# Performance work log

Hardware: AMD Instinct MI355X
Metric: run time of the kernel (lower is better)

Reference implementation:

```python
import jax, jax.numpy as jnp
import numpy as np

B = 2048   # batch
D = 1280   # backbone feature dim (hardcoded in module)
E = 8      # num_classes == number of expert heads
ALPHA = 0.1
EPS = 1e-5


def _bn(x, g, b, m, v):
    # BatchNorm1d in eval mode: running stats
    return (x - m) * jax.lax.rsqrt(v + EPS) * g + b


def _ln(x, g, b):
    mu = jnp.mean(x, axis=-1, keepdims=True)
    var = jnp.mean((x - mu) ** 2, axis=-1, keepdims=True)
    return (x - mu) * jax.lax.rsqrt(var + EPS) * g + b


@jax.custom_vjp
def _grad_reverse(x):
    return x

def _gr_fwd(x):
    return x, None

def _gr_bwd(_, g):
    return (-ALPHA * g,)

_grad_reverse.defvjp(_gr_fwd, _gr_bwd)


def setup_inputs() -> dict:
    key = jax.random.key(0)
    ks = iter(jax.random.split(key, 80))
    def w(*s):
        return jax.random.normal(next(ks), s, dtype=jnp.float32) * 0.02
    def u(*s):
        return jax.random.uniform(next(ks), s, dtype=jnp.float32) + 0.5
    inp = {"source": jax.random.normal(next(ks), (B, D), dtype=jnp.float32)}
    # bottleneck: Linear(1280,512)+BN+ReLU, Linear(512,256)+BN+ReLU
    inp.update(bw1=w(D, 512), bb1=jnp.zeros(512), bg1=jnp.ones(512), bbe1=jnp.zeros(512), bm1=w(512), bv1=u(512))
    inp.update(bw2=w(512, 256), bb2=jnp.zeros(256), bg2=jnp.ones(256), bbe2=jnp.zeros(256), bm2=w(256), bv2=u(256))
    # source_fc: Linear(256, E) + LogSoftmax
    inp.update(cw=w(256, E), cb=jnp.zeros(E))
    # domain classifier: 1280->1024->1024->512->2 with BN
    inp.update(dw1=w(D, 1024), db1=jnp.zeros(1024), dg1=jnp.ones(1024), dbe1=jnp.zeros(1024), dm1=w(1024), dv1=u(1024))
    inp.update(dw2=w(1024, 1024), db2=jnp.zeros(1024), dg2=jnp.ones(1024), dbe2=jnp.zeros(1024), dm2=w(1024), dv2=u(1024))
    inp.update(dw3=w(1024, 512), db3=jnp.zeros(512), dg3=jnp.ones(512), dbe3=jnp.zeros(512), dm3=w(512), dv3=u(512))
    inp.update(dw4=w(512, 2), db4=jnp.zeros(2))
    # E stacked expert MLPs: 1280->1024->1024->512->2 with LayerNorm
    inp.update(ew1=w(E, D, 1024), eb1=jnp.zeros((E, 1024)), eg1=jnp.ones((E, 1024)), ebe1=jnp.zeros((E, 1024)))
    inp.update(ew2=w(E, 1024, 1024), eb2=jnp.zeros((E, 1024)), eg2=jnp.ones((E, 1024)), ebe2=jnp.zeros((E, 1024)))
    inp.update(ew3=w(E, 1024, 512), eb3=jnp.zeros((E, 512)), eg3=jnp.ones((E, 512)), ebe3=jnp.zeros((E, 512)))
    inp.update(ew4=w(E, 512, 2), eb4=jnp.zeros((E, 2)))
    return inp


def reference(source, bw1, bb1, bg1, bbe1, bm1, bv1, bw2, bb2, bg2, bbe2, bm2, bv2, cw, cb,
              dw1, db1, dg1, dbe1, dm1, dv1, dw2, db2, dg2, dbe2, dm2, dv2,
              dw3, db3, dg3, dbe3, dm3, dv3, dw4, db4,
              ew1, eb1, eg1, ebe1, ew2, eb2, eg2, ebe2, ew3, eb3, eg3, ebe3, ew4, eb4):
    share = source  # sharedNet modeled as identity on extracted features
    # bottleneck + classifier head
    h = jax.nn.relu(_bn(share @ bw1 + bb1, bg1, bbe1, bm1, bv1))
    h = jax.nn.relu(_bn(h @ bw2 + bb2, bg2, bbe2, bm2, bv2))
    src = jax.nn.log_softmax(h @ cw + cb, axis=-1)            # [B, E]
    label = jnp.argmax(src, axis=-1)                          # routing labels (detached by argmax)
    # gradient-reversed features
    rev = _grad_reverse(share)
    # global domain classifier (dropout = identity in eval)
    d = jax.nn.relu(_bn(rev @ dw1 + db1, dg1, dbe1, dm1, dv1))
    d = jax.nn.relu(_bn(d @ dw2 + db2, dg2, dbe2, dm2, dv2))
    d = jax.nn.relu(_bn(d @ dw3 + db3, dg3, dbe3, dm3, dv3))
    dclf = jax.nn.log_softmax(d @ dw4 + db4, axis=-1)         # [B, 2]
    # per-class domain experts: dense all-expert compute + per-sample gather
    x = jax.nn.relu(_ln(jnp.einsum('bd,edh->beh', rev, ew1) + eb1[None], eg1[None], ebe1[None]))
    x = jax.nn.relu(_ln(jnp.einsum('beh,ehk->bek', x, ew2) + eb2[None], eg2[None], ebe2[None]))
    x = jax.nn.relu(_ln(jnp.einsum('beh,ehk->bek', x, ew3) + eb3[None], eg3[None], ebe3[None]))
    eo = jax.nn.log_softmax(jnp.einsum('beh,ehk->bek', x, ew4) + eb4[None], axis=-1)  # [B, E, 2]
    sout = jnp.take_along_axis(eo, label[:, None, None], axis=1)[:, 0, :]             # [B, 2]
    return (src, dclf, sout, share)
```

## Files before the change

### kernel.cpp

```cpp
#include <hip/hip_runtime.h>

typedef unsigned short u16;
typedef short s8v __attribute__((ext_vector_type(8)));
typedef float f4v __attribute__((ext_vector_type(4)));

#define AS1 __attribute__((address_space(1)))
#define AS3 __attribute__((address_space(3)))

__device__ __forceinline__ float bf2f(u16 u) {
    union { unsigned int i; float f; } x; x.i = ((unsigned int)u) << 16; return x.f;
}
__device__ __forceinline__ u16 f2bf(float f) {
    union { float f; unsigned int i; } x; x.f = f;
    unsigned int r = x.i + 0x7fffu + ((x.i >> 16) & 1u);
    return (u16)(r >> 16);
}

__device__ __forceinline__ void glds16(const u16* g, u16* l) {
    __builtin_amdgcn_global_load_lds((AS1 void*)(g), (AS3 void*)(l), 16, 0, 0);
}

__global__ __launch_bounds__(256) void convT_k(const float* __restrict__ W,
        u16* __restrict__ WT, int N, int K)
{
    const size_t mat = (size_t)blockIdx.z * K * N;
    const int n0 = blockIdx.x * 64, k0 = blockIdx.y * 64;
    __shared__ float t[64][65];
    const int r = threadIdx.x >> 2;
    const int c = (threadIdx.x & 3) << 4;
    const float* wp = W + mat + (size_t)(k0 + r) * N + n0 + c;
    #pragma unroll
    for (int q = 0; q < 16; q += 4) {
        float4 f = *(const float4*)(wp + q);
        t[c + q + 0][r] = f.x; t[c + q + 1][r] = f.y;
        t[c + q + 2][r] = f.z; t[c + q + 3][r] = f.w;
    }
    __syncthreads();
    u16* op = WT + mat + (size_t)(n0 + r) * K + k0 + c;
    #pragma unroll
    for (int q = 0; q < 16; q += 8) {
        s8v v;
        #pragma unroll
        for (int j = 0; j < 8; ++j) v[j] = (short)f2bf(t[r][c + q + j]);
        *(s8v*)(op + q) = v;
    }
}

__global__ __launch_bounds__(256) void conv_k(const float* __restrict__ in,
        u16* __restrict__ out, int n8)
{
    const int i = blockIdx.x * 256 + threadIdx.x;
    if (i >= n8) return;
    const float4 f0 = ((const float4*)in)[i * 2];
    const float4 f1 = ((const float4*)in)[i * 2 + 1];
    s8v v;
    v[0]=(short)f2bf(f0.x); v[1]=(short)f2bf(f0.y);
    v[2]=(short)f2bf(f0.z); v[3]=(short)f2bf(f0.w);
    v[4]=(short)f2bf(f1.x); v[5]=(short)f2bf(f1.y);
    v[6]=(short)f2bf(f1.z); v[7]=(short)f2bf(f1.w);
    ((s8v*)out)[i] = v;
}

template<int HASDOM>
__global__ __launch_bounds__(256) void gemm_bt128_k(
    const u16* __restrict__ A0, size_t aStrideZ,
    const u16* __restrict__ WT0,
    const float* __restrict__ ebias,
    const float* __restrict__ dbias, const float* __restrict__ dgam,
    const float* __restrict__ dbet,  const float* __restrict__ dmean,
    const float* __restrict__ dvar,  int zdom,
    u16* __restrict__ out0, int M, int N, int K)
{
    const int z = blockIdx.z;
    const u16* A  = A0  + (size_t)z * aStrideZ;
    const u16* WT = WT0 + (size_t)z * N * K;
    u16* out = out0 + (size_t)z * M * N;

    const int n0 = blockIdx.x * 128, m0 = blockIdx.y * 128;
    const int t = threadIdx.x;
    const int w = t >> 6, lane = t & 63;
    const int lq = lane >> 4, lr = lane & 15;
    const int wm = (w >> 1) * 64, wn = (w & 1) * 64;

    __shared__ __align__(16) u16 As[128 * 64];
    __shared__ __align__(16) u16 Bs[128 * 64];

    f4v acc[4][4] = {};

    const u16* ga = A  + (size_t)(m0 + (t >> 3)) * K + ((t & 7) << 3);
    const u16* gb = WT + (size_t)(n0 + (t >> 3)) * K + ((t & 7) << 3);
    const int ldsb = w * 512;

    for (int kk = 0; kk < K; kk += 64) {
        #pragma unroll
        for (int q = 0; q < 4; ++q) {
            glds16(ga + kk + (size_t)q * 32 * K, &As[q * 2048 + ldsb]);
            glds16(gb + kk + (size_t)q * 32 * K, &Bs[q * 2048 + ldsb]);
        }
        __syncthreads();
        #pragma unroll
        for (int ks = 0; ks < 64; ks += 32) {
            const int kq = ks + (lq << 3);
            s8v a[4], b[4];
            #pragma unroll
            for (int i = 0; i < 4; ++i) a[i] = *(const s8v*)&As[(wm + i*16 + lr) * 64 + kq];
            #pragma unroll
            for (int j = 0; j < 4; ++j) b[j] = *(const s8v*)&Bs[(wn + j*16 + lr) * 64 + kq];
            #pragma unroll
            for (int i = 0; i < 4; ++i)
                #pragma unroll
                for (int j = 0; j < 4; ++j)
                    acc[i][j] = __builtin_amdgcn_mfma_f32_16x16x32_bf16(a[i], b[j], acc[i][j], 0, 0, 0);
        }
        __syncthreads();
    }

    float scale[4], shift[4];
    const bool dom = HASDOM && (z == zdom);
    #pragma unroll
    for (int j = 0; j < 4; ++j) {
        const int c = n0 + wn + j * 16 + lr;
        if (dom) {
            const float s = dgam[c] / sqrtf(dvar[c] + 1e-5f);
            scale[j] = s;
            shift[j] = (dbias[c] - dmean[c]) * s + dbet[c];
        } else {
            scale[j] = 1.f;
            shift[j] = ebias[(size_t)z * N + c];
        }
    }
    const int r0 = lq << 2;
    #pragma unroll
    for (int i = 0; i < 4; ++i) {
        #pragma unroll
        for (int r = 0; r < 4; ++r) {
            const int grow = m0 + wm + i * 16 + r0 + r;
            u16* orow = out + (size_t)grow * N + n0 + wn + lr;
            #pragma unroll
            for (int j = 0; j < 4; ++j) {
                float y = fmaf(acc[i][j][r], scale[j], shift[j]);
                if (dom) y = fmaxf(y, 0.f);
                orow[j * 16] = f2bf(y);
            }
        }
    }
}

__global__ __launch_bounds__(256) void gemm_f32sk_k(
    const float* __restrict__ A, const float* __restrict__ W,
    float* __restrict__ out, int M, int N, int K, int Ks)
{
    const int n0 = blockIdx.x * 64, m0 = blockIdx.y * 64;
    const int kb = blockIdx.z * Ks;
    out += (size_t)blockIdx.z * M * N;
    const int tid = threadIdx.x;
    const int tx = tid & 15, ty = tid >> 4;
    __shared__ float As[64][65];
    __shared__ float Bs[64][64];
    float acc[4][4] = {};
    const int sr = tid >> 2;
    const int sc = (tid & 3) << 4;
    for (int kk = kb; kk < kb + Ks; kk += 64) {
        const float* ap = A + (size_t)(m0 + sr) * K + kk + sc;
        #pragma unroll
        for (int q = 0; q < 4; ++q) {
            float4 f = *(const float4*)(ap + q * 4);
            As[sr][sc + q*4 + 0] = f.x; As[sr][sc + q*4 + 1] = f.y;
            As[sr][sc + q*4 + 2] = f.z; As[sr][sc + q*4 + 3] = f.w;
        }
        const float* wp = W + (size_t)(kk + sr) * N + n0 + sc;
        #pragma unroll
        for (int q = 0; q < 4; ++q)
            *(float4*)&Bs[sr][sc + q*4] = *(const float4*)(wp + q * 4);
        __syncthreads();
        #pragma unroll 4
        for (int kq = 0; kq < 64; ++kq) {
            float a[4], bv[4];
            #pragma unroll
            for (int i = 0; i < 4; ++i) a[i] = As[ty*4 + i][kq];
            #pragma unroll
            for (int j = 0; j < 4; ++j) bv[j] = Bs[kq][tx*4 + j];
            #pragma unroll
            for (int i = 0; i < 4; ++i)
                #pragma unroll
                for (int j = 0; j < 4; ++j)
                    acc[i][j] = fmaf(a[i], bv[j], acc[i][j]);
        }
        __syncthreads();
    }
    #pragma unroll
    for (int j = 0; j < 4; ++j) {
        const int c = n0 + tx*4 + j;
        #pragma unroll
        for (int i = 0; i < 4; ++i)
            out[(size_t)(m0 + ty*4 + i) * N + c] = acc[i][j];
    }
}

__global__ __launch_bounds__(256) void h2cls_k(
    const float* __restrict__ hp,
    const float* __restrict__ bb1, const float* __restrict__ bg1,
    const float* __restrict__ bbe1, const float* __restrict__ bm1,
    const float* __restrict__ bv1,
    const float* __restrict__ bw2, const float* __restrict__ bb2,
    const float* __restrict__ bg2, const float* __restrict__ bbe2,
    const float* __restrict__ bm2, const float* __restrict__ bv2,
    const float* __restrict__ cw,  const float* __restrict__ cb,
    float* __restrict__ out_src, int* __restrict__ label, int B)
{
    const int b0 = blockIdx.x * 4;
    const int t = threadIdx.x;
    const size_t sl = (size_t)B * 512;
    __shared__ float h1s[4][512];
    __shared__ float h2s[4][256];

    #pragma unroll
    for (int cc = 0; cc < 2; ++cc) {
        const int c = t + cc * 256;
        const float sc = bg1[c] / sqrtf(bv1[c] + 1e-5f);
        const float sh = (bb1[c] - bm1[c]) * sc + bbe1[c];
        #pragma unroll
        for (int s = 0; s < 4; ++s) {
            const size_t ix = (size_t)(b0 + s) * 512 + c;
            const float v = hp[ix] + hp[ix + sl] + hp[ix + 2*sl] + hp[ix + 3*sl];
            h1s[s][c] = fmaxf(fmaf(v, sc, sh), 0.f);
        }
    }
    __syncthreads();

    float acc[4] = {};
    #pragma unroll 4
    for (int k = 0; k < 512; ++k) {
        const float wv = bw2[(size_t)k * 256 + t];
        #pragma unroll
        for (int s = 0; s < 4; ++s) acc[s] = fmaf(h1s[s][k], wv, acc[s]);
    }
    const float sc2 = bg2[t] / sqrtf(bv2[t] + 1e-5f);
    const float sh2 = (bb2[t] - bm2[t]) * sc2 + bbe2[t];
    #pragma unroll
    for (int s = 0; s < 4; ++s) h2s[s][t] = fmaxf(fmaf(acc[s], sc2, sh2), 0.f);
    __syncthreads();

    const int s = t >> 6, lane = t & 63;
    float p[8] = {};
    for (int k = lane; k < 256; k += 64) {
        const float x = h2s[s][k];
        #pragma unroll
        for (int c = 0; c < 8; ++c) p[c] = fmaf(x, cw[k * 8 + c], p[c]);
    }
    #pragma unroll
    for (int off = 32; off; off >>= 1)
        #pragma unroll
        for (int c = 0; c < 8; ++c) p[c] += __shfl_xor(p[c], off, 64);
    if (lane == 0) {
        const int b = b0 + s;
        float lg[8];
        #pragma unroll
        for (int c = 0; c < 8; ++c) lg[c] = p[c] + cb[c];
        float mx = lg[0]; int am = 0;
        #pragma unroll
        for (int c = 1; c < 8; ++c) if (lg[c] > mx) { mx = lg[c]; am = c; }
        float ssum = 0.f;
        #pragma unroll
        for (int c = 0; c < 8; ++c) ssum += expf(lg[c] - mx);
        const float lse = mx + logf(ssum);
        #pragma unroll
        for (int c = 0; c < 8; ++c) out_src[b * 8 + c] = lg[c] - lse;
        label[b] = am;
    }
}

template<int N>
__global__ __launch_bounds__(256) void ln_relu_k(u16* __restrict__ Y,
        const float* __restrict__ g, const float* __restrict__ bb)
{
    const int z = blockIdx.y;
    u16* y = Y + ((size_t)z * gridDim.x + blockIdx.x) * N;
    const float* gz = g  + (size_t)z * N;
    const float* bz = bb + (size_t)z * N;
    const int t = threadIdx.x;
    constexpr int C = N >> 8;
    float vals[C];
    if (C == 4) {
        ushort4 u = ((const ushort4*)y)[t];
        vals[0] = bf2f(u.x); vals[1] = bf2f(u.y);
        vals[2] = bf2f(u.z); vals[3] = bf2f(u.w);
    } else {
        ushort2 u = ((const ushort2*)y)[t];
        vals[0] = bf2f(u.x); vals[1] = bf2f(u.y);
    }
    float s = 0.f, sq = 0.f;
    #pragma unroll
    for (int i = 0; i < C; ++i) { s += vals[i]; sq += vals[i] * vals[i]; }
    #pragma unroll
    for (int off = 32; off; off >>= 1) {
        s  += __shfl_xor(s,  off, 64);
        sq += __shfl_xor(sq, off, 64);
    }
    __shared__ float rs[4], rq[4];
    if ((t & 63) == 0) { rs[t >> 6] = s; rq[t >> 6] = sq; }
    __syncthreads();
    s  = rs[0] + rs[1] + rs[2] + rs[3];
    sq = rq[0] + rq[1] + rq[2] + rq[3];
    const float inv = 1.f / (float)N;
    const float mu  = s * inv;
    const float var = sq * inv - mu * mu;
    const float rstd = rsqrtf(var + 1e-5f);
    if (C == 4) {
        float4 gv = ((const float4*)gz)[t];
        float4 bv = ((const float4*)bz)[t];
        ushort4 o;
        o.x = f2bf(fmaxf((vals[0] - mu) * rstd * gv.x + bv.x, 0.f));
        o.y = f2bf(fmaxf((vals[1] - mu) * rstd * gv.y + bv.y, 0.f));
        o.z = f2bf(fmaxf((vals[2] - mu) * rstd * gv.z + bv.z, 0.f));
        o.w = f2bf(fmaxf((vals[3] - mu) * rstd * gv.w + bv.w, 0.f));
        ((ushort4*)y)[t] = o;
    } else {
        float2 gv = ((const float2*)gz)[t];
        float2 bv = ((const float2*)bz)[t];
        ushort2 o;
        o.x = f2bf(fmaxf((vals[0] - mu) * rstd * gv.x + bv.x, 0.f));
        o.y = f2bf(fmaxf((vals[1] - mu) * rstd * gv.y + bv.y, 0.f));
        ((ushort2*)y)[t] = o;
    }
}

__global__ __launch_bounds__(64) void head2_k(const u16* __restrict__ X, size_t xsz,
        const float* __restrict__ W, size_t wsz,
        const float* __restrict__ bias, size_t bsz,
        int K, float* __restrict__ out, size_t osz)
{
    const int b = blockIdx.x, z = blockIdx.y;
    const int lane = threadIdx.x;
    const u16* x = X + z * xsz + (size_t)b * K;
    const float* Wz = W + z * wsz;
    const float* bz = bias + z * bsz;
    float* o = out + z * osz + (size_t)b * 2;
    float p0 = 0.f, p1 = 0.f;
    for (int k = lane; k < K; k += 64) {
        const float xv = bf2f(x[k]);
        p0 = fmaf(xv, Wz[k * 2],     p0);
        p1 = fmaf(xv, Wz[k * 2 + 1], p1);
    }
    #pragma unroll
    for (int off = 32; off; off >>= 1) {
        p0 += __shfl_xor(p0, off, 64);
        p1 += __shfl_xor(p1, off, 64);
    }
    if (lane == 0) {
        const float l0 = p0 + bz[0];
        const float l1 = p1 + bz[1];
        const float mx = fmaxf(l0, l1);
        const float lse = mx + logf(expf(l0 - mx) + expf(l1 - mx));
        o[0] = l0 - lse;
        o[1] = l1 - lse;
    }
}

__global__ __launch_bounds__(256) void gather_k(const float* __restrict__ eo,
        const int* __restrict__ label, float* __restrict__ out, int B)
{
    const int b = blockIdx.x * 256 + threadIdx.x;
    if (b >= B) return;
    const int e = label[b];
    out[b * 2]     = eo[((size_t)e * B + b) * 2];
    out[b * 2 + 1] = eo[((size_t)e * B + b) * 2 + 1];
}

__global__ __launch_bounds__(256) void copy16_k(const uint4* __restrict__ in,
                                                uint4* __restrict__ out, int n16)
{
    const int i = blockIdx.x * blockDim.x + threadIdx.x;
    if (i < n16) out[i] = in[i];
}


extern "C" void kernel_launch(void* const* d_in, const int* in_sizes, int n_in,
                              void* d_out, int out_size, void* d_ws, size_t ws_size,
                              hipStream_t stream)
{
    const int B = 2048, D = 1280, E = 8;

    const float* src = (const float*)d_in[0];
    const float *bw1 = (const float*)d_in[1],  *bb1 = (const float*)d_in[2],
                *bg1 = (const float*)d_in[3],  *bbe1 = (const float*)d_in[4],
                *bm1 = (const float*)d_in[5],  *bv1 = (const float*)d_in[6];
    const float *bw2 = (const float*)d_in[7],  *bb2 = (const float*)d_in[8],
                *bg2 = (const float*)d_in[9],  *bbe2 = (const float*)d_in[10],
                *bm2 = (const float*)d_in[11], *bv2 = (const float*)d_in[12];
    const float *cw  = (const float*)d_in[13], *cb  = (const float*)d_in[14];
    const float *dw1 = (const float*)d_in[15], *db1 = (const float*)d_in[16],
                *dg1 = (const float*)d_in[17], *dbe1 = (const float*)d_in[18],
                *dm1 = (const float*)d_in[19], *dv1 = (const float*)d_in[20];
    const float *dw2 = (const float*)d_in[21], *db2 = (const float*)d_in[22],
                *dg2 = (const float*)d_in[23], *dbe2 = (const float*)d_in[24],
                *dm2 = (const float*)d_in[25], *dv2 = (const float*)d_in[26];
    const float *dw3 = (const float*)d_in[27], *db3 = (const float*)d_in[28],
                *dg3 = (const float*)d_in[29], *dbe3 = (const float*)d_in[30],
                *dm3 = (const float*)d_in[31], *dv3 = (const float*)d_in[32];
    const float *dw4 = (const float*)d_in[33], *db4 = (const float*)d_in[34];
    const float *ew1 = (const float*)d_in[35], *eb1 = (const float*)d_in[36],
                *eg1 = (const float*)d_in[37], *ebe1 = (const float*)d_in[38];
    const float *ew2 = (const float*)d_in[39], *eb2 = (const float*)d_in[40],
                *eg2 = (const float*)d_in[41], *ebe2 = (const float*)d_in[42];
    const float *ew3 = (const float*)d_in[43], *eb3 = (const float*)d_in[44],
                *eg3 = (const float*)d_in[45], *ebe3 = (const float*)d_in[46];
    const float *ew4 = (const float*)d_in[47], *eb4 = (const float*)d_in[48];

    float* out_src   = (float*)d_out;
    float* out_dclf  = out_src + B * E;
    float* out_sout  = out_dclf + B * 2;
    float* out_share = out_sout + B * 2;

    char* ws = (char*)d_ws;
    u16*   wslot = (u16*)ws;
    u16*   srcb  = (u16*)(ws + 13107200);
    u16*   acta  = (u16*)(ws + 18350080);
    u16*   actb  = (u16*)(ws + 39321600);
    float* eo    = (float*)(ws + 60293120);
    int*   label = (int*)(ws + 60424192);
    float* hp    = (float*)(ws + 18350080);

    const size_t s1024 = (size_t)B * 1024, s512 = (size_t)B * 512;

    conv_k<<<dim3(B * D / 8 / 256), 256, 0, stream>>>(src, srcb, B * D / 8);
    copy16_k<<<dim3(B * D * 4 / 16 / 256), 256, 0, stream>>>(
        (const uint4*)src, (uint4*)out_share, B * D * 4 / 16);

    gemm_f32sk_k<<<dim3(512 / 64, B / 64, 4), 256, 0, stream>>>(
        src, bw1, hp, B, 512, D, 320);
    h2cls_k<<<dim3(B / 4), 256, 0, stream>>>(
        hp, bb1, bg1, bbe1, bm1, bv1, bw2, bb2, bg2, bbe2, bm2, bv2,
        cw, cb, out_src, label, B);

    convT_k<<<dim3(16, 20, 4), 256, 0, stream>>>(ew1, wslot, 1024, 1280);
    convT_k<<<dim3(16, 20, 1), 256, 0, stream>>>(dw1, wslot + (size_t)4*1024*1280, 1024, 1280);
    gemm_bt128_k<1><<<dim3(8, 16, 5), 256, 0, stream>>>(
        srcb, 0, wslot, eb1, db1, dg1, dbe1, dm1, dv1, 4, acta, B, 1024, 1280);
    ln_relu_k<1024><<<dim3(B, 4), 256, 0, stream>>>(acta, eg1, ebe1);

    convT_k<<<dim3(16, 16, 4), 256, 0, stream>>>(ew2, wslot, 1024, 1024);
    convT_k<<<dim3(16, 16, 1), 256, 0, stream>>>(dw2, wslot + (size_t)4*1024*1024, 1024, 1024);
    gemm_bt128_k<1><<<dim3(8, 16, 5), 256, 0, stream>>>(
        acta, s1024, wslot, eb2, db2, dg2, dbe2, dm2, dv2, 4, actb, B, 1024, 1024);
    ln_relu_k<1024><<<dim3(B, 4), 256, 0, stream>>>(actb, eg2, ebe2);

    convT_k<<<dim3(8, 16, 4), 256, 0, stream>>>(ew3, wslot, 512, 1024);
    convT_k<<<dim3(8, 16, 1), 256, 0, stream>>>(dw3, wslot + (size_t)4*512*1024, 512, 1024);
    gemm_bt128_k<1><<<dim3(4, 16, 5), 256, 0, stream>>>(
        actb, s1024, wslot, eb3, db3, dg3, dbe3, dm3, dv3, 4, acta, B, 512, 1024);
    ln_relu_k<512><<<dim3(B, 4), 256, 0, stream>>>(acta, eg3, ebe3);

    head2_k<<<dim3(B, 4), 64, 0, stream>>>(
        acta, s512, ew4, 1024, eb4, 2, 512, eo, (size_t)B * 2);
    head2_k<<<dim3(B, 1), 64, 0, stream>>>(
        acta + (size_t)4 * B * 512, 0, dw4, 0, db4, 0, 512, out_dclf, 0);

    convT_k<<<dim3(16, 20, 4), 256, 0, stream>>>(ew1 + (size_t)4*1280*1024, wslot, 1024, 1280);
    gemm_bt128_k<0><<<dim3(8, 16, 4), 256, 0, stream>>>(
        srcb, 0, wslot, eb1 + (size_t)4*1024,
        nullptr, nullptr, nullptr, nullptr, nullptr, -1, acta, B, 1024, 1280);
    ln_relu_k<1024><<<dim3(B, 4), 256, 0, stream>>>(acta, eg1 + (size_t)4*1024, ebe1 + (size_t)4*1024);

    convT_k<<<dim3(16, 16, 4), 256, 0, stream>>>(ew2 + (size_t)4*1024*1024, wslot, 1024, 1024);
    gemm_bt128_k<0><<<dim3(8, 16, 4), 256, 0, stream>>>(
        acta, s1024, wslot, eb2 + (size_t)4*1024,
        nullptr, nullptr, nullptr, nullptr, nullptr, -1, actb, B, 1024, 1024);
    ln_relu_k<1024><<<dim3(B, 4), 256, 0, stream>>>(actb, eg2 + (size_t)4*1024, ebe2 + (size_t)4*1024);

    convT_k<<<dim3(8, 16, 4), 256, 0, stream>>>(ew3 + (size_t)4*1024*512, wslot, 512, 1024);
    gemm_bt128_k<0><<<dim3(4, 16, 4), 256, 0, stream>>>(
        actb, s1024, wslot, eb3 + (size_t)4*512,
        nullptr, nullptr, nullptr, nullptr, nullptr, -1, acta, B, 512, 1024);
    ln_relu_k<512><<<dim3(B, 4), 256, 0, stream>>>(acta, eg3 + (size_t)4*512, ebe3 + (size_t)4*512);

    head2_k<<<dim3(B, 4), 64, 0, stream>>>(
        acta, s512, ew4 + (size_t)4*512*2, 1024, eb4 + 8, 2, 512,
        eo + (size_t)4 * B * 2, (size_t)B * 2);

    gather_k<<<dim3(B / 256), 256, 0, stream>>>(eo, label, out_sout, B);
}
```

Measured before the change: 669.9 us.

## Double-buffer GEMM LDS tiles with XOR swizzle and merge weight transpose launches

The bf16 MFMA GEMM now double-buffers its A/B shared-memory tiles. The next K-tile is prefetched via global_load_lds while the current tile is computed, and s_setprio raises wave priority around the MFMA block. LDS reads and writes use an XOR swizzle on 16-byte chunks to avoid bank conflicts. Separate expert and domain weight transpose kernels are merged into one launch via a z-split. The cost is double the LDS per block (64 KB), which may reduce occupancy.

```diff
diff --git a/kernel.cpp b/kernel.cpp
--- a/kernel.cpp
+++ b/kernel.cpp
@@ -20,15 +20,23 @@
     __builtin_amdgcn_global_load_lds((AS1 void*)(g), (AS3 void*)(l), 16, 0, 0);
 }
 
-__global__ __launch_bounds__(256) void convT_k(const float* __restrict__ W,
+__device__ __forceinline__ int swz(int row, int kq) {
+    return row * 64 + ((((kq >> 3) ^ row) & 7) << 3);
+}
+
+__global__ __launch_bounds__(256) void convT2_k(const float* __restrict__ Wa,
+        const float* __restrict__ Wb, int zSplit,
         u16* __restrict__ WT, int N, int K)
 {
-    const size_t mat = (size_t)blockIdx.z * K * N;
+    const int z = blockIdx.z;
+    const float* W = (z < zSplit) ? Wa + (size_t)z * K * N
+                                  : Wb + (size_t)(z - zSplit) * K * N;
+    WT += (size_t)z * K * N;
     const int n0 = blockIdx.x * 64, k0 = blockIdx.y * 64;
     __shared__ float t[64][65];
     const int r = threadIdx.x >> 2;
     const int c = (threadIdx.x & 3) << 4;
-    const float* wp = W + mat + (size_t)(k0 + r) * N + n0 + c;
+    const float* wp = W + (size_t)(k0 + r) * N + n0 + c;
     #pragma unroll
     for (int q = 0; q < 16; q += 4) {
         float4 f = *(const float4*)(wp + q);
@@ -36,7 +44,7 @@
         t[c + q + 2][r] = f.z; t[c + q + 3][r] = f.w;
     }
     __syncthreads();
-    u16* op = WT + mat + (size_t)(n0 + r) * K + k0 + c;
+    u16* op = WT + (size_t)(n0 + r) * K + k0 + c;
     #pragma unroll
     for (int q = 0; q < 16; q += 8) {
         s8v v;
@@ -61,6 +69,16 @@
     ((s8v*)out)[i] = v;
 }
 
+__device__ __forceinline__ void stage_tile(u16* AsH, u16* BsH,
+        const u16* ga, const u16* gb, int kk, int ldsq, int K)
+{
+    #pragma unroll
+    for (int q = 0; q < 4; ++q) {
+        glds16(ga + kk + (size_t)q * 32 * K, AsH + q * 2048 + ldsq);
+        glds16(gb + kk + (size_t)q * 32 * K, BsH + q * 2048 + ldsq);
+    }
+}
+
 template<int HASDOM>
 __global__ __launch_bounds__(256) void gemm_bt128_k(
     const u16* __restrict__ A0, size_t aStrideZ,
@@ -82,37 +100,45 @@
     const int lq = lane >> 4, lr = lane & 15;
     const int wm = (w >> 1) * 64, wn = (w & 1) * 64;
 
-    __shared__ __align__(16) u16 As[128 * 64];
-    __shared__ __align__(16) u16 Bs[128 * 64];
+    __shared__ __align__(16) u16 As[2 * 128 * 64];
+    __shared__ __align__(16) u16 Bs[2 * 128 * 64];
 
     f4v acc[4][4] = {};
 
-    const u16* ga = A  + (size_t)(m0 + (t >> 3)) * K + ((t & 7) << 3);
-    const u16* gb = WT + (size_t)(n0 + (t >> 3)) * K + ((t & 7) << 3);
-    const int ldsb = w * 512;
-
-    for (int kk = 0; kk < K; kk += 64) {
-        #pragma unroll
-        for (int q = 0; q < 4; ++q) {
-            glds16(ga + kk + (size_t)q * 32 * K, &As[q * 2048 + ldsb]);
-            glds16(gb + kk + (size_t)q * 32 * K, &Bs[q * 2048 + ldsb]);
-        }
-        __syncthreads();
+    const int schunk = ((t & 7) ^ ((t >> 3) & 7)) << 3;
+    const u16* ga = A  + (size_t)(m0 + (t >> 3)) * K + schunk;
+    const u16* gb = WT + (size_t)(n0 + (t >> 3)) * K + schunk;
+    const int ldsq = w * 512;
+
+    const int NT = K >> 6;
+    int cur = 0;
+    stage_tile(As, Bs, ga, gb, 0, ldsq, K);
+    __syncthreads();
+
+    for (int tk = 0; tk < NT; ++tk) {
+        if (tk + 1 < NT)
+            stage_tile(As + (cur ^ 1) * 8192, Bs + (cur ^ 1) * 8192,
+                       ga, gb, (tk + 1) << 6, ldsq, K);
+        const u16* Ah = As + cur * 8192;
+        const u16* Bh = Bs + cur * 8192;
+        __builtin_amdgcn_s_setprio(1);
         #pragma unroll
         for (int ks = 0; ks < 64; ks += 32) {
             const int kq = ks + (lq << 3);
             s8v a[4], b[4];
             #pragma unroll
-            for (int i = 0; i < 4; ++i) a[i] = *(const s8v*)&As[(wm + i*16 + lr) * 64 + kq];
-            #pragma unroll
-            for (int j = 0; j < 4; ++j) b[j] = *(const s8v*)&Bs[(wn + j*16 + lr) * 64 + kq];
+            for (int i = 0; i < 4; ++i) a[i] = *(const s8v*)&Ah[swz(wm + i*16 + lr, kq)];
+            #pragma unroll
+            for (int j = 0; j < 4; ++j) b[j] = *(const s8v*)&Bh[swz(wn + j*16 + lr, kq)];
             #pragma unroll
             for (int i = 0; i < 4; ++i)
                 #pragma unroll
                 for (int j = 0; j < 4; ++j)
                     acc[i][j] = __builtin_amdgcn_mfma_f32_16x16x32_bf16(a[i], b[j], acc[i][j], 0, 0, 0);
         }
+        __builtin_amdgcn_s_setprio(0);
         __syncthreads();
+        cur ^= 1;
     }
 
     float scale[4], shift[4];
@@ -433,20 +459,17 @@
         hp, bb1, bg1, bbe1, bm1, bv1, bw2, bb2, bg2, bbe2, bm2, bv2,
         cw, cb, out_src, label, B);
 
-    convT_k<<<dim3(16, 20, 4), 256, 0, stream>>>(ew1, wslot, 1024, 1280);
-    convT_k<<<dim3(16, 20, 1), 256, 0, stream>>>(dw1, wslot + (size_t)4*1024*1280, 1024, 1280);
+    convT2_k<<<dim3(16, 20, 5), 256, 0, stream>>>(ew1, dw1, 4, wslot, 1024, 1280);
     gemm_bt128_k<1><<<dim3(8, 16, 5), 256, 0, stream>>>(
         srcb, 0, wslot, eb1, db1, dg1, dbe1, dm1, dv1, 4, acta, B, 1024, 1280);
     ln_relu_k<1024><<<dim3(B, 4), 256, 0, stream>>>(acta, eg1, ebe1);
 
-    convT_k<<<dim3(16, 16, 4), 256, 0, stream>>>(ew2, wslot, 1024, 1024);
-    convT_k<<<dim3(16, 16, 1), 256, 0, stream>>>(dw2, wslot + (size_t)4*1024*1024, 1024, 1024);
+    convT2_k<<<dim3(16, 16, 5), 256, 0, stream>>>(ew2, dw2, 4, wslot, 1024, 1024);
     gemm_bt128_k<1><<<dim3(8, 16, 5), 256, 0, stream>>>(
         acta, s1024, wslot, eb2, db2, dg2, dbe2, dm2, dv2, 4, actb, B, 1024, 1024);
     ln_relu_k<1024><<<dim3(B, 4), 256, 0, stream>>>(actb, eg2, ebe2);
 
-    convT_k<<<dim3(8, 16, 4), 256, 0, stream>>>(ew3, wslot, 512, 1024);
-    convT_k<<<dim3(8, 16, 1), 256, 0, stream>>>(dw3, wslot + (size_t)4*512*1024, 512, 1024);
+    convT2_k<<<dim3(8, 16, 5), 256, 0, stream>>>(ew3, dw3, 4, wslot, 512, 1024);
     gemm_bt128_k<1><<<dim3(4, 16, 5), 256, 0, stream>>>(
         actb, s1024, wslot, eb3, db3, dg3, dbe3, dm3, dv3, 4, acta, B, 512, 1024);
     ln_relu_k<512><<<dim3(B, 4), 256, 0, stream>>>(acta, eg3, ebe3);
@@ -456,19 +479,22 @@
     head2_k<<<dim3(B, 1), 64, 0, stream>>>(
         acta + (size_t)4 * B * 512, 0, dw4, 0, db4, 0, 512, out_dclf, 0);
 
-    convT_k<<<dim3(16, 20, 4), 256, 0, stream>>>(ew1 + (size_t)4*1280*1024, wslot, 1024, 1280);
+    convT2_k<<<dim3(16, 20, 4), 256, 0, stream>>>(
+        ew1 + (size_t)4*1280*1024, ew1 + (size_t)4*1280*1024, 4, wslot, 1024, 1280);
     gemm_bt128_k<0><<<dim3(8, 16, 4), 256, 0, stream>>>(
         srcb, 0, wslot, eb1 + (size_t)4*1024,
         nullptr, nullptr, nullptr, nullptr, nullptr, -1, acta, B, 1024, 1280);
     ln_relu_k<1024><<<dim3(B, 4), 256, 0, stream>>>(acta, eg1 + (size_t)4*1024, ebe1 + (size_t)4*1024);
 
-    convT_k<<<dim3(16, 16, 4), 256, 0, stream>>>(ew2 + (size_t)4*1024*1024, wslot, 1024, 1024);
+    convT2_k<<<dim3(16, 16, 4), 256, 0, stream>>>(
+        ew2 + (size_t)4*1024*1024, ew2 + (size_t)4*1024*1024, 4, wslot, 1024, 1024);
     gemm_bt128_k<0><<<dim3(8, 16, 4), 256, 0, stream>>>(
         acta, s1024, wslot, eb2 + (size_t)4*1024,
         nullptr, nullptr, nullptr, nullptr, nullptr, -1, actb, B, 1024, 1024);
     ln_relu_k<1024><<<dim3(B, 4), 256, 0, stream>>>(actb, eg2 + (size_t)4*1024, ebe2 + (size_t)4*1024);
 
-    convT_k<<<dim3(8, 16, 4), 256, 0, stream>>>(ew3 + (size_t)4*1024*512, wslot, 512, 1024);
+    convT2_k<<<dim3(8, 16, 4), 256, 0, stream>>>(
+        ew3 + (size_t)4*1024*512, ew3 + (size_t)4*1024*512, 4, wslot, 512, 1024);
     gemm_bt128_k<0><<<dim3(4, 16, 4), 256, 0, stream>>>(
         actb, s1024, wslot, eb3 + (size_t)4*512,
         nullptr, nullptr, nullptr, nullptr, nullptr, -1, acta, B, 512, 1024);
```

Measured after the change: 620.9 us. 1.08x faster.
